# Kernel optimization log

Hardware: AMD Instinct MI355X
Metric: run time of the kernel (lower is better)

Reference implementation:

```python
import jax, jax.numpy as jnp
import numpy as np

W = 8       # token width
H = 2       # attention heads
NC = 1024   # number of cycles
L = 256     # darts per cycle
CLAMP = 10000.0


def _safe(x, clamp=CLAMP):
    x = jnp.nan_to_num(x, nan=0.0, posinf=clamp, neginf=-clamp)
    return jnp.clip(x, -clamp, clamp)


def _safe_softmax(logits, axis):
    w = jax.nn.softmax(_safe(logits), axis=axis)
    w = jnp.nan_to_num(w, nan=0.0, posinf=0.0, neginf=0.0)
    denom = jnp.maximum(w.sum(axis=axis, keepdims=True), 1e-6)
    return w / denom


def _layernorm(x, g, b, eps=1e-5):
    mu = x.mean(-1, keepdims=True)
    var = x.var(-1, keepdims=True)  # biased, matches torch LayerNorm
    return (x - mu) * jax.lax.rsqrt(var + eps) * g + b


def _mha(x, in_w, in_b, out_w, out_b, n_heads, mask=None):
    # torch nn.MultiheadAttention (batch_first) semantics. x: [B,S,E]
    B, S, E = x.shape
    d = E // n_heads
    qkv = x @ in_w.T + in_b
    q, k, v = jnp.split(qkv, 3, axis=-1)
    q = q.reshape(B, S, n_heads, d)
    k = k.reshape(B, S, n_heads, d)
    v = v.reshape(B, S, n_heads, d)
    scores = jnp.einsum('bshd,bthd->bhst', q, k) / jnp.sqrt(jnp.asarray(d, x.dtype))
    if mask is not None:
        scores = scores + mask  # broadcast [S,S] over batch/heads
    attn = jax.nn.softmax(scores, axis=-1)
    out = jnp.einsum('bhst,bthd->bshd', attn, v).reshape(B, S, E)
    return out @ out_w.T + out_b


def _cycle_mask(length):
    m = jnp.full((length, length), -1e9, dtype=jnp.float32)
    i = jnp.arange(length)
    m = m.at[i, i].set(0.0)
    m = m.at[i, (i - 1) % length].set(0.0)
    m = m.at[i, (i + 1) % length].set(0.0)
    return m


def _normalize_orientation(darts):
    # darts: [L,2]; polygon vertices are cumulative sums (origin first, last dart dropped)
    verts = jnp.concatenate([jnp.zeros((1, 2), darts.dtype), jnp.cumsum(darts[:-1], axis=0)], axis=0)
    x, y = verts[:, 0], verts[:, 1]
    area = 0.5 * jnp.sum(x * jnp.roll(y, -1) - y * jnp.roll(x, -1))
    return jnp.where(area >= 0.0, darts, jnp.flip(-darts, axis=0))


def setup_inputs() -> dict:
    key = jax.random.key(0)
    ks = jax.random.split(key, 32)
    def p(i, shape, s=0.2):
        return jax.random.normal(ks[i], shape, jnp.float32) * s
    return {
        'dart_features': jax.random.normal(ks[0], (NC, L, 3), jnp.float32),
        # dart_embed Linear(3,W)
        'de_w': p(1, (W, 3)), 'de_b': p(2, (W,)),
        # cycle_attn MultiheadAttention(W, 2)
        'ca_in_w': p(3, (3 * W, W)), 'ca_in_b': p(4, (3 * W,)),
        'ca_out_w': p(5, (W, W)), 'ca_out_b': p(6, (W,)),
        # cycle_norm
        'cn_g': jnp.ones((W,), jnp.float32), 'cn_b': jnp.zeros((W,), jnp.float32),
        # cycle_score Linear(W,1)
        'cs_w': p(7, (1, W)), 'cs_b': p(8, (1,)),
        # cycle_pool_proj: LN, Linear, ReLU, Linear
        'cp_ln_g': jnp.ones((W,), jnp.float32), 'cp_ln_b': jnp.zeros((W,), jnp.float32),
        'cp_w1': p(9, (W, W)), 'cp_b1': p(10, (W,)),
        'cp_w2': p(11, (W, W)), 'cp_b2': p(12, (W,)),
        # inter_cycle_attn
        'ia_in_w': p(13, (3 * W, W)), 'ia_in_b': p(14, (3 * W,)),
        'ia_out_w': p(15, (W, W)), 'ia_out_b': p(16, (W,)),
        # inter_cycle_norm
        'in_g': jnp.ones((W,), jnp.float32), 'in_b': jnp.zeros((W,), jnp.float32),
        # inter_cycle_score
        'is_w': p(17, (1, W)), 'is_b': p(18, (1,)),
        # token_proj: LN, Linear, ReLU, Linear
        'tp_ln_g': jnp.ones((W,), jnp.float32), 'tp_ln_b': jnp.zeros((W,), jnp.float32),
        'tp_w1': p(19, (W, W)), 'tp_b1': p(20, (W,)),
        'tp_w2': p(21, (W, W)), 'tp_b2': p(22, (W,)),
    }


def reference(dart_features, de_w, de_b, ca_in_w, ca_in_b, ca_out_w, ca_out_b,
              cn_g, cn_b, cs_w, cs_b, cp_ln_g, cp_ln_b, cp_w1, cp_b1, cp_w2, cp_b2,
              ia_in_w, ia_in_b, ia_out_w, ia_out_b, in_g, in_b, is_w, is_b,
              tp_ln_g, tp_ln_b, tp_w1, tp_b1, tp_w2, tp_b2):
    nc, ln, _ = dart_features.shape
    # ---- encode_cycle, vectorized over all cycles ----
    xy = jax.vmap(_normalize_orientation)(dart_features[..., :2])          # [C,L,2]
    nrm = jnp.linalg.norm(xy, axis=-1, keepdims=True)
    feats = _safe(jnp.concatenate([xy, nrm], axis=-1))                     # [C,L,3]
    emb = _safe(jax.nn.relu(feats @ de_w.T + de_b))                        # [C,L,W]
    mask = _cycle_mask(ln)
    attn = _mha(emb, ca_in_w, ca_in_b, ca_out_w, ca_out_b, H, mask)
    emb = _safe(_layernorm(_safe(emb + attn), cn_g, cn_b))                 # [C,L,W]
    logits = _safe((emb @ cs_w.T + cs_b)[..., 0])                          # [C,L]
    wts = _safe_softmax(logits, axis=1)
    pooled = jnp.sum(emb * wts[..., None], axis=1)                         # [C,W]
    hpool = _layernorm(pooled, cp_ln_g, cp_ln_b)
    cyc = _safe(jax.nn.relu(hpool @ cp_w1.T + cp_b1) @ cp_w2.T + cp_b2)    # [C,W]
    # ---- tokenize_collection ----
    coll = _safe(cyc)[None]                                                # [1,C,W]
    attn2 = _mha(coll, ia_in_w, ia_in_b, ia_out_w, ia_out_b, H)
    coll = _safe(_layernorm(_safe(coll + attn2), in_g, in_b))[0]           # [C,W]
    lg = _safe((coll @ is_w.T + is_b)[..., 0])                             # [C]
    w2 = _safe_softmax(lg, axis=0)
    tok_in = jnp.sum(coll * w2[:, None], axis=0)                           # [W]
    h2 = _layernorm(tok_in, tp_ln_g, tp_ln_b)
    token = _safe(jax.nn.relu(h2 @ tp_w1.T + tp_b1) @ tp_w2.T + tp_b2)     # [W]
    return token
```

## Files before the change

### kernel.cpp

```cpp
#include <hip/hip_runtime.h>
#include <math.h>

#define FCLAMP 10000.0f
#define NCYC 1024
#define NB2 (NCYC / 4)

__device__ __forceinline__ float safef(float x) {
    if (isnan(x)) return 0.0f;
    return fmaxf(fminf(x, FCLAMP), -FCLAMP);
}

__device__ __forceinline__ float wsum_b(float v) {
#pragma unroll
    for (int m = 1; m <= 32; m <<= 1) v += __shfl_xor(v, m, 64);
    return v;
}
__device__ __forceinline__ float wmax_b(float v) {
#pragma unroll
    for (int m = 1; m <= 32; m <<= 1) v = fmaxf(v, __shfl_xor(v, m, 64));
    return v;
}

__global__ __launch_bounds__(64, 1) void k_cycle(
    const float* __restrict__ df,
    const float* __restrict__ de_w, const float* __restrict__ de_b,
    const float* __restrict__ ca_in_w, const float* __restrict__ ca_in_b,
    const float* __restrict__ ca_out_w, const float* __restrict__ ca_out_b,
    const float* __restrict__ cn_g, const float* __restrict__ cn_b,
    const float* __restrict__ cs_w, const float* __restrict__ cs_b,
    const float* __restrict__ cp_ln_g, const float* __restrict__ cp_ln_b,
    const float* __restrict__ cp_w1, const float* __restrict__ cp_b1,
    const float* __restrict__ cp_w2, const float* __restrict__ cp_b2,
    const float* __restrict__ ia_in_w, const float* __restrict__ ia_in_b,
    float* __restrict__ ws_cyc,
    float* __restrict__ ws_q,
    float* __restrict__ ws_kT,
    float* __restrict__ ws_vT,
    unsigned* __restrict__ ws_cnt)
{
    const int lane = threadIdx.x;
    const int nc   = blockIdx.x;
    if (nc == 0 && lane == 0) *ws_cnt = 0u;

    const float* base = df + (size_t)nc * 768 + lane * 12;
    const float4 A = *(const float4*)(base);
    const float4 B = *(const float4*)(base + 4);
    const float4 C = *(const float4*)(base + 8);
    float dxr[4] = {A.x, A.w, B.z, C.y};
    float dyr[4] = {A.y, B.x, B.w, C.z};

    float sx[4], sy[4];
    sx[0] = dxr[0]; sy[0] = dyr[0];
#pragma unroll
    for (int r = 1; r < 4; ++r) { sx[r] = sx[r - 1] + dxr[r]; sy[r] = sy[r - 1] + dyr[r]; }
    const float tx = sx[3], ty = sy[3];
    float ixs = tx, iys = ty;
#pragma unroll
    for (int off = 1; off < 64; off <<= 1) {
        const float ax = __shfl_up(ixs, off, 64);
        const float ay = __shfl_up(iys, off, 64);
        if (lane >= off) { ixs += ax; iys += ay; }
    }
    const float bx = ixs - tx, by = iys - ty;

    float cc = 0.f;
#pragma unroll
    for (int r = 0; r < 4; ++r) {
        const float vx = bx + (r ? sx[r - 1] : 0.f);
        const float vy = by + (r ? sy[r - 1] : 0.f);
        if ((lane * 4 + r) < 255) cc += vx * dyr[r] - vy * dxr[r];
    }
    const float area2 = wsum_b(cc);

    if (!(area2 >= 0.f)) {
        float nx[4], ny[4];
#pragma unroll
        for (int r = 0; r < 4; ++r) {
            nx[r] = -__shfl(dxr[3 - r], 63 - lane, 64);
            ny[r] = -__shfl(dyr[3 - r], 63 - lane, 64);
        }
#pragma unroll
        for (int r = 0; r < 4; ++r) { dxr[r] = nx[r]; dyr[r] = ny[r]; }
    }

    float embA[4][8];
#pragma unroll
    for (int r = 0; r < 4; ++r) {
        const float fx = safef(dxr[r]);
        const float fy = safef(dyr[r]);
        const float fn = safef(sqrtf(dxr[r] * dxr[r] + dyr[r] * dyr[r]));
#pragma unroll
        for (int j = 0; j < 8; ++j) {
            const float e = de_b[j] + fx * de_w[j * 3] + fy * de_w[j * 3 + 1] + fn * de_w[j * 3 + 2];
            embA[r][j] = safef(fmaxf(e, 0.f));
        }
    }

    float qA[4][8], kA[4][8], vA[4][8];
#pragma unroll
    for (int r = 0; r < 4; ++r) {
#pragma unroll
        for (int o = 0; o < 24; ++o) {
            float val = ca_in_b[o];
#pragma unroll
            for (int k = 0; k < 8; ++k) val += embA[r][k] * ca_in_w[o * 8 + k];
            if (o < 8)       qA[r][o] = val;
            else if (o < 16) kA[r][o - 8] = val;
            else             vA[r][o - 16] = val;
        }
    }

    const int lprev = (lane + 63) & 63, lnext = (lane + 1) & 63;
    float kp[8], kn[8], vp[8], vn[8];
#pragma unroll
    for (int d = 0; d < 8; ++d) {
        kp[d] = __shfl(kA[3][d], lprev, 64);
        kn[d] = __shfl(kA[0][d], lnext, 64);
        vp[d] = __shfl(vA[3][d], lprev, 64);
        vn[d] = __shfl(vA[0][d], lnext, 64);
    }

    float lgr[4];
#pragma unroll
    for (int r = 0; r < 4; ++r) {
        float kprev[8], knext[8], vprev[8], vnext[8];
#pragma unroll
        for (int d = 0; d < 8; ++d) {
            kprev[d] = (r == 0) ? kp[d] : kA[r - 1][d];
            knext[d] = (r == 3) ? kn[d] : kA[r + 1][d];
            vprev[d] = (r == 0) ? vp[d] : vA[r - 1][d];
            vnext[d] = (r == 3) ? vn[d] : vA[r + 1][d];
        }
        float att[8];
#pragma unroll
        for (int h = 0; h < 2; ++h) {
            float s0 = 0.f, s1 = 0.f, s2 = 0.f;
#pragma unroll
            for (int d = 0; d < 4; ++d) {
                const float qv = qA[r][h * 4 + d];
                s0 += qv * kprev[h * 4 + d];
                s1 += qv * kA[r][h * 4 + d];
                s2 += qv * knext[h * 4 + d];
            }
            s0 *= 0.5f; s1 *= 0.5f; s2 *= 0.5f;
            const float m  = fmaxf(s0, fmaxf(s1, s2));
            const float e0 = __expf(s0 - m), e1 = __expf(s1 - m), e2 = __expf(s2 - m);
            const float inv = 1.f / (e0 + e1 + e2);
#pragma unroll
            for (int d = 0; d < 4; ++d)
                att[h * 4 + d] = (e0 * vprev[h * 4 + d] + e1 * vA[r][h * 4 + d] +
                                  e2 * vnext[h * 4 + d]) * inv;
        }
        float x8[8];
#pragma unroll
        for (int j = 0; j < 8; ++j) {
            float ao = ca_out_b[j];
#pragma unroll
            for (int k = 0; k < 8; ++k) ao += att[k] * ca_out_w[j * 8 + k];
            x8[j] = safef(embA[r][j] + ao);
        }
        float mu = 0.f;
#pragma unroll
        for (int j = 0; j < 8; ++j) mu += x8[j];
        mu *= 0.125f;
        float var = 0.f;
#pragma unroll
        for (int j = 0; j < 8; ++j) { const float d = x8[j] - mu; var += d * d; }
        var *= 0.125f;
        const float rs = rsqrtf(var + 1e-5f);
        float lg = cs_b[0];
#pragma unroll
        for (int j = 0; j < 8; ++j) {
            embA[r][j] = safef((x8[j] - mu) * rs * cn_g[j] + cn_b[j]);
            lg += embA[r][j] * cs_w[j];
        }
        lgr[r] = safef(lg);
    }

    float M = fmaxf(fmaxf(lgr[0], lgr[1]), fmaxf(lgr[2], lgr[3]));
    M = wmax_b(M);
    float er[4], esum = 0.f;
#pragma unroll
    for (int r = 0; r < 4; ++r) { er[r] = __expf(lgr[r] - M); esum += er[r]; }
    const float S = wsum_b(esum);
    const float invS = 1.f / S;
    float pool[8];
#pragma unroll
    for (int j = 0; j < 8; ++j) {
        float pj = er[0] * embA[0][j] + er[1] * embA[1][j] + er[2] * embA[2][j] + er[3] * embA[3][j];
        pool[j] = wsum_b(pj) * invS;
    }

    float mu2 = 0.f;
#pragma unroll
    for (int j = 0; j < 8; ++j) mu2 += pool[j];
    mu2 *= 0.125f;
    float v2 = 0.f;
#pragma unroll
    for (int j = 0; j < 8; ++j) { const float d = pool[j] - mu2; v2 += d * d; }
    const float rs2 = rsqrtf(v2 * 0.125f + 1e-5f);
    float hh[8];
#pragma unroll
    for (int j = 0; j < 8; ++j) hh[j] = (pool[j] - mu2) * rs2 * cp_ln_g[j] + cp_ln_b[j];
    float r1[8];
#pragma unroll
    for (int j = 0; j < 8; ++j) {
        float a = cp_b1[j];
#pragma unroll
        for (int k = 0; k < 8; ++k) a += hh[k] * cp_w1[j * 8 + k];
        r1[j] = fmaxf(a, 0.f);
    }
    float cy[8];
#pragma unroll
    for (int j = 0; j < 8; ++j) {
        float a = cp_b2[j];
#pragma unroll
        for (int k = 0; k < 8; ++k) a += r1[k] * cp_w2[j * 8 + k];
        cy[j] = safef(a);
    }
    if (lane == 0) {
        *(float4*)(ws_cyc + nc * 8)     = make_float4(cy[0], cy[1], cy[2], cy[3]);
        *(float4*)(ws_cyc + nc * 8 + 4) = make_float4(cy[4], cy[5], cy[6], cy[7]);
    }

    if (lane < 24) {
        const float* wrow = ia_in_w + lane * 8;
        float g2 = ia_in_b[lane];
#pragma unroll
        for (int k = 0; k < 8; ++k) g2 += cy[k] * wrow[k];
        if (lane < 8)       ws_q[nc * 8 + lane] = g2;
        else if (lane < 16) ws_kT[(lane - 8) * NCYC + nc] = g2;
        else                ws_vT[(lane - 16) * NCYC + nc] = g2;
    }
}

__global__ __launch_bounds__(256) void k_attn_final(
    const float* __restrict__ ws_cyc,
    const float* __restrict__ ws_q,
    const float* __restrict__ ws_kT,
    const float* __restrict__ ws_vT,
    const float* __restrict__ ia_out_w, const float* __restrict__ ia_out_b,
    const float* __restrict__ in_g, const float* __restrict__ in_b,
    const float* __restrict__ is_w, const float* __restrict__ is_b,
    const float* __restrict__ tp_ln_g, const float* __restrict__ tp_ln_b,
    const float* __restrict__ tp_w1, const float* __restrict__ tp_b1,
    const float* __restrict__ tp_w2, const float* __restrict__ tp_b2,
    float* __restrict__ ws_coll,
    float* __restrict__ ws_lg,
    unsigned* __restrict__ ws_cnt,
    float* __restrict__ out)
{
    __shared__ float sredM[4], sredS[4], spool[4][8];
    __shared__ unsigned s_last;

    const int lane = threadIdx.x & 63;
    const int wid  = threadIdx.x >> 6;
    const int g    = blockIdx.x * 4 + wid;

    float q[8];
#pragma unroll
    for (int d = 0; d < 8; ++d) q[d] = 0.5f * ws_q[g * 8 + d];

    float sc0[16], sc1[16];
    float m0 = -1e30f, m1 = -1e30f;
#pragma unroll
    for (int j = 0; j < 4; ++j) {
        const int t4 = j * 256 + lane * 4;
        float s0[4] = {0, 0, 0, 0}, s1[4] = {0, 0, 0, 0};
#pragma unroll
        for (int d = 0; d < 8; ++d) {
            const float4 kv = *(const float4*)(ws_kT + d * NCYC + t4);
            const float qd = q[d];
            float* s = (d < 4) ? s0 : s1;
            s[0] += qd * kv.x; s[1] += qd * kv.y; s[2] += qd * kv.z; s[3] += qd * kv.w;
        }
#pragma unroll
        for (int c = 0; c < 4; ++c) {
            sc0[j * 4 + c] = s0[c]; sc1[j * 4 + c] = s1[c];
            m0 = fmaxf(m0, s0[c]); m1 = fmaxf(m1, s1[c]);
        }
    }
    m0 = wmax_b(m0); m1 = wmax_b(m1);

    float l0 = 0.f, l1 = 0.f;
    float a0[4] = {0, 0, 0, 0}, a1[4] = {0, 0, 0, 0};
#pragma unroll
    for (int j = 0; j < 4; ++j) {
        const int t4 = j * 256 + lane * 4;
        float e0[4], e1[4];
#pragma unroll
        for (int c = 0; c < 4; ++c) {
            e0[c] = __expf(sc0[j * 4 + c] - m0);
            e1[c] = __expf(sc1[j * 4 + c] - m1);
            l0 += e0[c]; l1 += e1[c];
        }
#pragma unroll
        for (int d = 0; d < 4; ++d) {
            const float4 v0 = *(const float4*)(ws_vT + d * NCYC + t4);
            const float4 v1 = *(const float4*)(ws_vT + (4 + d) * NCYC + t4);
            a0[d] += e0[0] * v0.x + e0[1] * v0.y + e0[2] * v0.z + e0[3] * v0.w;
            a1[d] += e1[0] * v1.x + e1[1] * v1.y + e1[2] * v1.z + e1[3] * v1.w;
        }
    }
    l0 = wsum_b(l0); l1 = wsum_b(l1);
#pragma unroll
    for (int d = 0; d < 4; ++d) { a0[d] = wsum_b(a0[d]); a1[d] = wsum_b(a1[d]); }

    float attn8[8];
#pragma unroll
    for (int d = 0; d < 4; ++d) { attn8[d] = a0[d] / l0; attn8[4 + d] = a1[d] / l1; }

    const float4 cyA = *(const float4*)(ws_cyc + g * 8);
    const float4 cyB = *(const float4*)(ws_cyc + g * 8 + 4);
    const float cyc[8] = {cyA.x, cyA.y, cyA.z, cyA.w, cyB.x, cyB.y, cyB.z, cyB.w};
    float x8[8];
#pragma unroll
    for (int j = 0; j < 8; ++j) {
        float ao = ia_out_b[j];
#pragma unroll
        for (int k = 0; k < 8; ++k) ao += attn8[k] * ia_out_w[j * 8 + k];
        x8[j] = safef(cyc[j] + ao);
    }
    float mu = 0.f;
#pragma unroll
    for (int j = 0; j < 8; ++j) mu += x8[j];
    mu *= 0.125f;
    float var = 0.f;
#pragma unroll
    for (int j = 0; j < 8; ++j) { const float d = x8[j] - mu; var += d * d; }
    var *= 0.125f;
    const float rs = rsqrtf(var + 1e-5f);
    float lgv = is_b[0];
    float cl8[8];
#pragma unroll
    for (int j = 0; j < 8; ++j) {
        cl8[j] = safef((x8[j] - mu) * rs * in_g[j] + in_b[j]);
        lgv += cl8[j] * is_w[j];
    }
    if (lane == 0) {
        *(float4*)(ws_coll + g * 8)     = make_float4(cl8[0], cl8[1], cl8[2], cl8[3]);
        *(float4*)(ws_coll + g * 8 + 4) = make_float4(cl8[4], cl8[5], cl8[6], cl8[7]);
        ws_lg[g] = safef(lgv);
    }

    __syncthreads();
    if (threadIdx.x == 0) {
        __threadfence();
        const unsigned old = atomicAdd(ws_cnt, 1u);
        s_last = (old == NB2 - 1) ? 1u : 0u;
    }
    __syncthreads();
    if (!s_last) return;
    __threadfence();

    const int tid = threadIdx.x;
    float lgv4[4], cl[4][8];
#pragma unroll
    for (int r = 0; r < 4; ++r) {
        const int t = tid + 256 * r;
        lgv4[r] = ws_lg[t];
        const float4 u = *(const float4*)(ws_coll + t * 8);
        const float4 w = *(const float4*)(ws_coll + t * 8 + 4);
        cl[r][0] = u.x; cl[r][1] = u.y; cl[r][2] = u.z; cl[r][3] = u.w;
        cl[r][4] = w.x; cl[r][5] = w.y; cl[r][6] = w.z; cl[r][7] = w.w;
    }
    float m = fmaxf(fmaxf(lgv4[0], lgv4[1]), fmaxf(lgv4[2], lgv4[3]));
    m = wmax_b(m);
    if (lane == 0) sredM[wid] = m;
    __syncthreads();
    const float M = fmaxf(fmaxf(sredM[0], sredM[1]), fmaxf(sredM[2], sredM[3]));
    float er[4], es = 0.f;
#pragma unroll
    for (int r = 0; r < 4; ++r) { er[r] = __expf(lgv4[r] - M); es += er[r]; }
    es = wsum_b(es);
    if (lane == 0) sredS[wid] = es;
#pragma unroll
    for (int j = 0; j < 8; ++j) {
        float pj = er[0] * cl[0][j] + er[1] * cl[1][j] + er[2] * cl[2][j] + er[3] * cl[3][j];
        pj = wsum_b(pj);
        if (lane == 0) spool[wid][j] = pj;
    }
    __syncthreads();

    if (wid == 0) {
        const float S = sredS[0] + sredS[1] + sredS[2] + sredS[3];
        const float invS = 1.f / S;
        float pool[8];
#pragma unroll
        for (int j = 0; j < 8; ++j)
            pool[j] = (spool[0][j] + spool[1][j] + spool[2][j] + spool[3][j]) * invS;
        float mu2 = 0.f;
#pragma unroll
        for (int j = 0; j < 8; ++j) mu2 += pool[j];
        mu2 *= 0.125f;
        float v2 = 0.f;
#pragma unroll
        for (int j = 0; j < 8; ++j) { const float d = pool[j] - mu2; v2 += d * d; }
        const float rs2 = rsqrtf(v2 * 0.125f + 1e-5f);
        float hh[8];
#pragma unroll
        for (int j = 0; j < 8; ++j) hh[j] = (pool[j] - mu2) * rs2 * tp_ln_g[j] + tp_ln_b[j];
        float r1[8];
#pragma unroll
        for (int j = 0; j < 8; ++j) {
            float a = tp_b1[j];
#pragma unroll
            for (int k = 0; k < 8; ++k) a += hh[k] * tp_w1[j * 8 + k];
            r1[j] = fmaxf(a, 0.f);
        }
        if (lane == 0) {
#pragma unroll
            for (int j = 0; j < 8; ++j) {
                float a = tp_b2[j];
#pragma unroll
                for (int k = 0; k < 8; ++k) a += r1[k] * tp_w2[j * 8 + k];
                out[j] = safef(a);
            }
        }
    }
}

extern "C" void kernel_launch(void* const* d_in, const int* in_sizes, int n_in,
                              void* d_out, int out_size, void* d_ws, size_t ws_size,
                              hipStream_t stream) {
    const float* df       = (const float*)d_in[0];
    const float* de_w     = (const float*)d_in[1];
    const float* de_b     = (const float*)d_in[2];
    const float* ca_in_w  = (const float*)d_in[3];
    const float* ca_in_b  = (const float*)d_in[4];
    const float* ca_out_w = (const float*)d_in[5];
    const float* ca_out_b = (const float*)d_in[6];
    const float* cn_g     = (const float*)d_in[7];
    const float* cn_b     = (const float*)d_in[8];
    const float* cs_w     = (const float*)d_in[9];
    const float* cs_b     = (const float*)d_in[10];
    const float* cp_ln_g  = (const float*)d_in[11];
    const float* cp_ln_b  = (const float*)d_in[12];
    const float* cp_w1    = (const float*)d_in[13];
    const float* cp_b1    = (const float*)d_in[14];
    const float* cp_w2    = (const float*)d_in[15];
    const float* cp_b2    = (const float*)d_in[16];
    const float* ia_in_w  = (const float*)d_in[17];
    const float* ia_in_b  = (const float*)d_in[18];
    const float* ia_out_w = (const float*)d_in[19];
    const float* ia_out_b = (const float*)d_in[20];
    const float* in_g     = (const float*)d_in[21];
    const float* in_b     = (const float*)d_in[22];
    const float* is_w     = (const float*)d_in[23];
    const float* is_b     = (const float*)d_in[24];
    const float* tp_ln_g  = (const float*)d_in[25];
    const float* tp_ln_b  = (const float*)d_in[26];
    const float* tp_w1    = (const float*)d_in[27];
    const float* tp_b1    = (const float*)d_in[28];
    const float* tp_w2    = (const float*)d_in[29];
    const float* tp_b2    = (const float*)d_in[30];

    float* ws      = (float*)d_ws;
    float* ws_cyc  = ws;
    float* ws_q    = ws + NCYC * 8;
    float* ws_kT   = ws + NCYC * 16;
    float* ws_vT   = ws + NCYC * 24;
    float* ws_coll = ws + NCYC * 32;
    float* ws_lg   = ws + NCYC * 40;
    unsigned* ws_cnt = (unsigned*)(ws + NCYC * 41);

    k_cycle<<<NCYC, 64, 0, stream>>>(
        df, de_w, de_b, ca_in_w, ca_in_b, ca_out_w, ca_out_b,
        cn_g, cn_b, cs_w, cs_b, cp_ln_g, cp_ln_b,
        cp_w1, cp_b1, cp_w2, cp_b2, ia_in_w, ia_in_b,
        ws_cyc, ws_q, ws_kT, ws_vT, ws_cnt);

    k_attn_final<<<NB2, 256, 0, stream>>>(
        ws_cyc, ws_q, ws_kT, ws_vT, ia_out_w, ia_out_b, in_g, in_b, is_w, is_b,
        tp_ln_g, tp_ln_b, tp_w1, tp_b1, tp_w2, tp_b2,
        ws_coll, ws_lg, ws_cnt, (float*)d_out);
}
```

Measured before the change: 149.0 us.

## Fuse both stages into one cooperative kernel with grid syncs

Merges the per-cycle kernel and the collection-attention/final-reduction kernel into a single cooperative launch of 1024 single-wave blocks. Two grid-wide barriers replace the second kernel launch and the atomic last-block counter. The collection attention is now computed by one 64-lane wave per query instead of the previous 256-thread blocks, and block 0 alone does the final softmax pooling and MLP. This removes one launch boundary but adds grid-sync costs and requires all 1024 blocks to be co-resident.

After: 391.5 us. 163% more time.

```diff
diff --git a/kernel.cpp b/kernel.cpp
--- a/kernel.cpp
+++ b/kernel.cpp
@@ -1,9 +1,11 @@
 #include <hip/hip_runtime.h>
+#include <hip/hip_cooperative_groups.h>
 #include <math.h>
+
+namespace cg = cooperative_groups;
 
 #define FCLAMP 10000.0f
 #define NCYC 1024
-#define NB2 (NCYC / 4)
 
 __device__ __forceinline__ float safef(float x) {
     if (isnan(x)) return 0.0f;
@@ -21,143 +23,297 @@
     return v;
 }
 
-__global__ __launch_bounds__(64, 1) void k_cycle(
-    const float* __restrict__ df,
-    const float* __restrict__ de_w, const float* __restrict__ de_b,
-    const float* __restrict__ ca_in_w, const float* __restrict__ ca_in_b,
-    const float* __restrict__ ca_out_w, const float* __restrict__ ca_out_b,
-    const float* __restrict__ cn_g, const float* __restrict__ cn_b,
-    const float* __restrict__ cs_w, const float* __restrict__ cs_b,
-    const float* __restrict__ cp_ln_g, const float* __restrict__ cp_ln_b,
-    const float* __restrict__ cp_w1, const float* __restrict__ cp_b1,
-    const float* __restrict__ cp_w2, const float* __restrict__ cp_b2,
-    const float* __restrict__ ia_in_w, const float* __restrict__ ia_in_b,
-    float* __restrict__ ws_cyc,
-    float* __restrict__ ws_q,
-    float* __restrict__ ws_kT,
-    float* __restrict__ ws_vT,
-    unsigned* __restrict__ ws_cnt)
-{
+struct Params {
+    const float* df;
+    const float* de_w;  const float* de_b;
+    const float* ca_in_w;  const float* ca_in_b;
+    const float* ca_out_w; const float* ca_out_b;
+    const float* cn_g;  const float* cn_b;
+    const float* cs_w;  const float* cs_b;
+    const float* cp_ln_g; const float* cp_ln_b;
+    const float* cp_w1; const float* cp_b1;
+    const float* cp_w2; const float* cp_b2;
+    const float* ia_in_w;  const float* ia_in_b;
+    const float* ia_out_w; const float* ia_out_b;
+    const float* in_g;  const float* in_b;
+    const float* is_w;  const float* is_b;
+    const float* tp_ln_g; const float* tp_ln_b;
+    const float* tp_w1; const float* tp_b1;
+    const float* tp_w2; const float* tp_b2;
+    float* ws_cyc;
+    float* ws_q;
+    float* ws_kT;
+    float* ws_vT;
+    float* ws_coll;
+    float* ws_lg;
+    float* out;
+};
+
+__global__ __launch_bounds__(64, 1) void k_all(Params p) {
     const int lane = threadIdx.x;
     const int nc   = blockIdx.x;
-    if (nc == 0 && lane == 0) *ws_cnt = 0u;
-
-    const float* base = df + (size_t)nc * 768 + lane * 12;
-    const float4 A = *(const float4*)(base);
-    const float4 B = *(const float4*)(base + 4);
-    const float4 C = *(const float4*)(base + 8);
-    float dxr[4] = {A.x, A.w, B.z, C.y};
-    float dyr[4] = {A.y, B.x, B.w, C.z};
-
-    float sx[4], sy[4];
-    sx[0] = dxr[0]; sy[0] = dyr[0];
-#pragma unroll
-    for (int r = 1; r < 4; ++r) { sx[r] = sx[r - 1] + dxr[r]; sy[r] = sy[r - 1] + dyr[r]; }
-    const float tx = sx[3], ty = sy[3];
-    float ixs = tx, iys = ty;
-#pragma unroll
-    for (int off = 1; off < 64; off <<= 1) {
-        const float ax = __shfl_up(ixs, off, 64);
-        const float ay = __shfl_up(iys, off, 64);
-        if (lane >= off) { ixs += ax; iys += ay; }
+
+    {
+        const float* base = p.df + (size_t)nc * 768 + lane * 12;
+        const float4 A = *(const float4*)(base);
+        const float4 B = *(const float4*)(base + 4);
+        const float4 C = *(const float4*)(base + 8);
+        float dxr[4] = {A.x, A.w, B.z, C.y};
+        float dyr[4] = {A.y, B.x, B.w, C.z};
+
+        float sx[4], sy[4];
+        sx[0] = dxr[0]; sy[0] = dyr[0];
+#pragma unroll
+        for (int r = 1; r < 4; ++r) { sx[r] = sx[r - 1] + dxr[r]; sy[r] = sy[r - 1] + dyr[r]; }
+        const float tx = sx[3], ty = sy[3];
+        float ixs = tx, iys = ty;
+#pragma unroll
+        for (int off = 1; off < 64; off <<= 1) {
+            const float ax = __shfl_up(ixs, off, 64);
+            const float ay = __shfl_up(iys, off, 64);
+            if (lane >= off) { ixs += ax; iys += ay; }
+        }
+        const float bx = ixs - tx, by = iys - ty;
+
+        float cc = 0.f;
+#pragma unroll
+        for (int r = 0; r < 4; ++r) {
+            const float vx = bx + (r ? sx[r - 1] : 0.f);
+            const float vy = by + (r ? sy[r - 1] : 0.f);
+            if ((lane * 4 + r) < 255) cc += vx * dyr[r] - vy * dxr[r];
+        }
+        const float area2 = wsum_b(cc);
+
+        if (!(area2 >= 0.f)) {
+            float nx[4], ny[4];
+#pragma unroll
+            for (int r = 0; r < 4; ++r) {
+                nx[r] = -__shfl(dxr[3 - r], 63 - lane, 64);
+                ny[r] = -__shfl(dyr[3 - r], 63 - lane, 64);
+            }
+#pragma unroll
+            for (int r = 0; r < 4; ++r) { dxr[r] = nx[r]; dyr[r] = ny[r]; }
+        }
+
+        float embA[4][8];
+#pragma unroll
+        for (int r = 0; r < 4; ++r) {
+            const float fx = safef(dxr[r]);
+            const float fy = safef(dyr[r]);
+            const float fn = safef(sqrtf(dxr[r] * dxr[r] + dyr[r] * dyr[r]));
+#pragma unroll
+            for (int j = 0; j < 8; ++j) {
+                const float e = p.de_b[j] + fx * p.de_w[j * 3] + fy * p.de_w[j * 3 + 1]
+                              + fn * p.de_w[j * 3 + 2];
+                embA[r][j] = safef(fmaxf(e, 0.f));
+            }
+        }
+
+        float qA[4][8], kA[4][8], vA[4][8];
+#pragma unroll
+        for (int r = 0; r < 4; ++r) {
+#pragma unroll
+            for (int o = 0; o < 24; ++o) {
+                float val = p.ca_in_b[o];
+#pragma unroll
+                for (int k = 0; k < 8; ++k) val += embA[r][k] * p.ca_in_w[o * 8 + k];
+                if (o < 8)       qA[r][o] = val;
+                else if (o < 16) kA[r][o - 8] = val;
+                else             vA[r][o - 16] = val;
+            }
+        }
+
+        const int lprev = (lane + 63) & 63, lnext = (lane + 1) & 63;
+        float kp[8], kn[8], vp[8], vn[8];
+#pragma unroll
+        for (int d = 0; d < 8; ++d) {
+            kp[d] = __shfl(kA[3][d], lprev, 64);
+            kn[d] = __shfl(kA[0][d], lnext, 64);
+            vp[d] = __shfl(vA[3][d], lprev, 64);
+            vn[d] = __shfl(vA[0][d], lnext, 64);
+        }
+
+        float lgr[4];
+#pragma unroll
+        for (int r = 0; r < 4; ++r) {
+            float kprev[8], knext[8], vprev[8], vnext[8];
+#pragma unroll
+            for (int d = 0; d < 8; ++d) {
+                kprev[d] = (r == 0) ? kp[d] : kA[r - 1][d];
+                knext[d] = (r == 3) ? kn[d] : kA[r + 1][d];
+                vprev[d] = (r == 0) ? vp[d] : vA[r - 1][d];
+                vnext[d] = (r == 3) ? vn[d] : vA[r + 1][d];
+            }
+            float att[8];
+#pragma unroll
+            for (int h = 0; h < 2; ++h) {
+                float s0 = 0.f, s1 = 0.f, s2 = 0.f;
+#pragma unroll
+                for (int d = 0; d < 4; ++d) {
+                    const float qv = qA[r][h * 4 + d];
+                    s0 += qv * kprev[h * 4 + d];
+                    s1 += qv * kA[r][h * 4 + d];
+                    s2 += qv * knext[h * 4 + d];
+                }
+                s0 *= 0.5f; s1 *= 0.5f; s2 *= 0.5f;
+                const float m  = fmaxf(s0, fmaxf(s1, s2));
+                const float e0 = __expf(s0 - m), e1 = __expf(s1 - m), e2 = __expf(s2 - m);
+                const float inv = 1.f / (e0 + e1 + e2);
+#pragma unroll
+                for (int d = 0; d < 4; ++d)
+                    att[h * 4 + d] = (e0 * vprev[h * 4 + d] + e1 * vA[r][h * 4 + d] +
+                                      e2 * vnext[h * 4 + d]) * inv;
+            }
+            float x8[8];
+#pragma unroll
+            for (int j = 0; j < 8; ++j) {
+                float ao = p.ca_out_b[j];
+#pragma unroll
+                for (int k = 0; k < 8; ++k) ao += att[k] * p.ca_out_w[j * 8 + k];
+                x8[j] = safef(embA[r][j] + ao);
+            }
+            float mu = 0.f;
+#pragma unroll
+            for (int j = 0; j < 8; ++j) mu += x8[j];
+            mu *= 0.125f;
+            float var = 0.f;
+#pragma unroll
+            for (int j = 0; j < 8; ++j) { const float d = x8[j] - mu; var += d * d; }
+            var *= 0.125f;
+            const float rs = rsqrtf(var + 1e-5f);
+            float lg = p.cs_b[0];
+#pragma unroll
+            for (int j = 0; j < 8; ++j) {
+                embA[r][j] = safef((x8[j] - mu) * rs * p.cn_g[j] + p.cn_b[j]);
+                lg += embA[r][j] * p.cs_w[j];
+            }
+            lgr[r] = safef(lg);
+        }
+
+        float M = fmaxf(fmaxf(lgr[0], lgr[1]), fmaxf(lgr[2], lgr[3]));
+        M = wmax_b(M);
+        float er[4], esum = 0.f;
+#pragma unroll
+        for (int r = 0; r < 4; ++r) { er[r] = __expf(lgr[r] - M); esum += er[r]; }
+        const float S = wsum_b(esum);
+        const float invS = 1.f / S;
+        float pool[8];
+#pragma unroll
+        for (int j = 0; j < 8; ++j) {
+            float pj = er[0] * embA[0][j] + er[1] * embA[1][j]
+                     + er[2] * embA[2][j] + er[3] * embA[3][j];
+            pool[j] = wsum_b(pj) * invS;
+        }
+
+        float mu2 = 0.f;
+#pragma unroll
+        for (int j = 0; j < 8; ++j) mu2 += pool[j];
+        mu2 *= 0.125f;
+        float v2 = 0.f;
+#pragma unroll
+        for (int j = 0; j < 8; ++j) { const float d = pool[j] - mu2; v2 += d * d; }
+        const float rs2 = rsqrtf(v2 * 0.125f + 1e-5f);
+        float hh[8];
+#pragma unroll
+        for (int j = 0; j < 8; ++j) hh[j] = (pool[j] - mu2) * rs2 * p.cp_ln_g[j] + p.cp_ln_b[j];
+        float r1[8];
+#pragma unroll
+        for (int j = 0; j < 8; ++j) {
+            float a = p.cp_b1[j];
+#pragma unroll
+            for (int k = 0; k < 8; ++k) a += hh[k] * p.cp_w1[j * 8 + k];
+            r1[j] = fmaxf(a, 0.f);
+        }
+        float cy[8];
+#pragma unroll
+        for (int j = 0; j < 8; ++j) {
+            float a = p.cp_b2[j];
+#pragma unroll
+            for (int k = 0; k < 8; ++k) a += r1[k] * p.cp_w2[j * 8 + k];
+            cy[j] = safef(a);
+        }
+        if (lane == 0) {
+            *(float4*)(p.ws_cyc + nc * 8)     = make_float4(cy[0], cy[1], cy[2], cy[3]);
+            *(float4*)(p.ws_cyc + nc * 8 + 4) = make_float4(cy[4], cy[5], cy[6], cy[7]);
+        }
+        if (lane < 24) {
+            const float* wrow = p.ia_in_w + lane * 8;
+            float g2 = p.ia_in_b[lane];
+#pragma unroll
+            for (int k = 0; k < 8; ++k) g2 += cy[k] * wrow[k];
+            if (lane < 8)       p.ws_q[nc * 8 + lane] = g2;
+            else if (lane < 16) p.ws_kT[(lane - 8) * NCYC + nc] = g2;
+            else                p.ws_vT[(lane - 16) * NCYC + nc] = g2;
+        }
     }
-    const float bx = ixs - tx, by = iys - ty;
-
-    float cc = 0.f;
-#pragma unroll
-    for (int r = 0; r < 4; ++r) {
-        const float vx = bx + (r ? sx[r - 1] : 0.f);
-        const float vy = by + (r ? sy[r - 1] : 0.f);
-        if ((lane * 4 + r) < 255) cc += vx * dyr[r] - vy * dxr[r];
-    }
-    const float area2 = wsum_b(cc);
-
-    if (!(area2 >= 0.f)) {
-        float nx[4], ny[4];
-#pragma unroll
-        for (int r = 0; r < 4; ++r) {
-            nx[r] = -__shfl(dxr[3 - r], 63 - lane, 64);
-            ny[r] = -__shfl(dyr[3 - r], 63 - lane, 64);
-        }
-#pragma unroll
-        for (int r = 0; r < 4; ++r) { dxr[r] = nx[r]; dyr[r] = ny[r]; }
-    }
-
-    float embA[4][8];
-#pragma unroll
-    for (int r = 0; r < 4; ++r) {
-        const float fx = safef(dxr[r]);
-        const float fy = safef(dyr[r]);
-        const float fn = safef(sqrtf(dxr[r] * dxr[r] + dyr[r] * dyr[r]));
-#pragma unroll
-        for (int j = 0; j < 8; ++j) {
-            const float e = de_b[j] + fx * de_w[j * 3] + fy * de_w[j * 3 + 1] + fn * de_w[j * 3 + 2];
-            embA[r][j] = safef(fmaxf(e, 0.f));
-        }
-    }
-
-    float qA[4][8], kA[4][8], vA[4][8];
-#pragma unroll
-    for (int r = 0; r < 4; ++r) {
-#pragma unroll
-        for (int o = 0; o < 24; ++o) {
-            float val = ca_in_b[o];
-#pragma unroll
-            for (int k = 0; k < 8; ++k) val += embA[r][k] * ca_in_w[o * 8 + k];
-            if (o < 8)       qA[r][o] = val;
-            else if (o < 16) kA[r][o - 8] = val;
-            else             vA[r][o - 16] = val;
-        }
-    }
-
-    const int lprev = (lane + 63) & 63, lnext = (lane + 1) & 63;
-    float kp[8], kn[8], vp[8], vn[8];
-#pragma unroll
-    for (int d = 0; d < 8; ++d) {
-        kp[d] = __shfl(kA[3][d], lprev, 64);
-        kn[d] = __shfl(kA[0][d], lnext, 64);
-        vp[d] = __shfl(vA[3][d], lprev, 64);
-        vn[d] = __shfl(vA[0][d], lnext, 64);
-    }
-
-    float lgr[4];
-#pragma unroll
-    for (int r = 0; r < 4; ++r) {
-        float kprev[8], knext[8], vprev[8], vnext[8];
-#pragma unroll
-        for (int d = 0; d < 8; ++d) {
-            kprev[d] = (r == 0) ? kp[d] : kA[r - 1][d];
-            knext[d] = (r == 3) ? kn[d] : kA[r + 1][d];
-            vprev[d] = (r == 0) ? vp[d] : vA[r - 1][d];
-            vnext[d] = (r == 3) ? vn[d] : vA[r + 1][d];
-        }
-        float att[8];
-#pragma unroll
-        for (int h = 0; h < 2; ++h) {
-            float s0 = 0.f, s1 = 0.f, s2 = 0.f;
+
+    cg::this_grid().sync();
+
+    {
+        const int g = nc;
+        float q[8];
+#pragma unroll
+        for (int d = 0; d < 8; ++d) q[d] = 0.5f * p.ws_q[g * 8 + d];
+
+        float sc0[16], sc1[16];
+        float m0 = -1e30f, m1 = -1e30f;
+#pragma unroll
+        for (int j = 0; j < 4; ++j) {
+            const int t4 = j * 256 + lane * 4;
+            float s0[4] = {0, 0, 0, 0}, s1[4] = {0, 0, 0, 0};
+#pragma unroll
+            for (int d = 0; d < 8; ++d) {
+                const float4 kv = *(const float4*)(p.ws_kT + d * NCYC + t4);
+                const float qd = q[d];
+                float* s = (d < 4) ? s0 : s1;
+                s[0] += qd * kv.x; s[1] += qd * kv.y; s[2] += qd * kv.z; s[3] += qd * kv.w;
+            }
+#pragma unroll
+            for (int c = 0; c < 4; ++c) {
+                sc0[j * 4 + c] = s0[c]; sc1[j * 4 + c] = s1[c];
+                m0 = fmaxf(m0, s0[c]); m1 = fmaxf(m1, s1[c]);
+            }
+        }
+        m0 = wmax_b(m0); m1 = wmax_b(m1);
+
+        float l0 = 0.f, l1 = 0.f;
+        float a0[4] = {0, 0, 0, 0}, a1[4] = {0, 0, 0, 0};
+#pragma unroll
+        for (int j = 0; j < 4; ++j) {
+            const int t4 = j * 256 + lane * 4;
+            float e0[4], e1[4];
+#pragma unroll
+            for (int c = 0; c < 4; ++c) {
+                e0[c] = __expf(sc0[j * 4 + c] - m0);
+                e1[c] = __expf(sc1[j * 4 + c] - m1);
+                l0 += e0[c]; l1 += e1[c];
+            }
 #pragma unroll
             for (int d = 0; d < 4; ++d) {
-                const float qv = qA[r][h * 4 + d];
-                s0 += qv * kprev[h * 4 + d];
-                s1 += qv * kA[r][h * 4 + d];
-                s2 += qv * knext[h * 4 + d];
-            }
-            s0 *= 0.5f; s1 *= 0.5f; s2 *= 0.5f;
-            const float m  = fmaxf(s0, fmaxf(s1, s2));
-            const float e0 = __expf(s0 - m), e1 = __expf(s1 - m), e2 = __expf(s2 - m);
-            const float inv = 1.f / (e0 + e1 + e2);
-#pragma unroll
-            for (int d = 0; d < 4; ++d)
-                att[h * 4 + d] = (e0 * vprev[h * 4 + d] + e1 * vA[r][h * 4 + d] +
-                                  e2 * vnext[h * 4 + d]) * inv;
-        }
+                const float4 v0 = *(const float4*)(p.ws_vT + d * NCYC + t4);
+                const float4 v1 = *(const float4*)(p.ws_vT + (4 + d) * NCYC + t4);
+                a0[d] += e0[0] * v0.x + e0[1] * v0.y + e0[2] * v0.z + e0[3] * v0.w;
+                a1[d] += e1[0] * v1.x + e1[1] * v1.y + e1[2] * v1.z + e1[3] * v1.w;
+            }
+        }
+        l0 = wsum_b(l0); l1 = wsum_b(l1);
+#pragma unroll
+        for (int d = 0; d < 4; ++d) { a0[d] = wsum_b(a0[d]); a1[d] = wsum_b(a1[d]); }
+
+        float attn8[8];
+#pragma unroll
+        for (int d = 0; d < 4; ++d) { attn8[d] = a0[d] / l0; attn8[4 + d] = a1[d] / l1; }
+
+        const float4 cyA = *(const float4*)(p.ws_cyc + g * 8);
+        const float4 cyB = *(const float4*)(p.ws_cyc + g * 8 + 4);
+        const float cyc[8] = {cyA.x, cyA.y, cyA.z, cyA.w, cyB.x, cyB.y, cyB.z, cyB.w};
         float x8[8];
 #pragma unroll
         for (int j = 0; j < 8; ++j) {
-            float ao = ca_out_b[j];
-#pragma unroll
-            for (int k = 0; k < 8; ++k) ao += att[k] * ca_out_w[j * 8 + k];
-            x8[j] = safef(embA[r][j] + ao);
+            float ao = p.ia_out_b[j];
+#pragma unroll
+            for (int k = 0; k < 8; ++k) ao += attn8[k] * p.ia_out_w[j * 8 + k];
+            x8[j] = safef(cyc[j] + ao);
         }
         float mu = 0.f;
 #pragma unroll
@@ -168,227 +324,49 @@
         for (int j = 0; j < 8; ++j) { const float d = x8[j] - mu; var += d * d; }
         var *= 0.125f;
         const float rs = rsqrtf(var + 1e-5f);
-        float lg = cs_b[0];
-#pragma unroll
-        for (int j = 0; j < 8; ++j) {
-            embA[r][j] = safef((x8[j] - mu) * rs * cn_g[j] + cn_b[j]);
-            lg += embA[r][j] * cs_w[j];
-        }
-        lgr[r] = safef(lg);
+        float lgv = p.is_b[0];
+        float cl8[8];
+#pragma unroll
+        for (int j = 0; j < 8; ++j) {
+            cl8[j] = safef((x8[j] - mu) * rs * p.in_g[j] + p.in_b[j]);
+            lgv += cl8[j] * p.is_w[j];
+        }
+        if (lane == 0) {
+            *(float4*)(p.ws_coll + g * 8)     = make_float4(cl8[0], cl8[1], cl8[2], cl8[3]);
+            *(float4*)(p.ws_coll + g * 8 + 4) = make_float4(cl8[4], cl8[5], cl8[6], cl8[7]);
+            p.ws_lg[g] = safef(lgv);
+        }
     }
 
-    float M = fmaxf(fmaxf(lgr[0], lgr[1]), fmaxf(lgr[2], lgr[3]));
-    M = wmax_b(M);
-    float er[4], esum = 0.f;
-#pragma unroll
-    for (int r = 0; r < 4; ++r) { er[r] = __expf(lgr[r] - M); esum += er[r]; }
-    const float S = wsum_b(esum);
-    const float invS = 1.f / S;
-    float pool[8];
-#pragma unroll
-    for (int j = 0; j < 8; ++j) {
-        float pj = er[0] * embA[0][j] + er[1] * embA[1][j] + er[2] * embA[2][j] + er[3] * embA[3][j];
-        pool[j] = wsum_b(pj) * invS;
-    }
-
-    float mu2 = 0.f;
-#pragma unroll
-    for (int j = 0; j < 8; ++j) mu2 += pool[j];
-    mu2 *= 0.125f;
-    float v2 = 0.f;
-#pragma unroll
-    for (int j = 0; j < 8; ++j) { const float d = pool[j] - mu2; v2 += d * d; }
-    const float rs2 = rsqrtf(v2 * 0.125f + 1e-5f);
-    float hh[8];
-#pragma unroll
-    for (int j = 0; j < 8; ++j) hh[j] = (pool[j] - mu2) * rs2 * cp_ln_g[j] + cp_ln_b[j];
-    float r1[8];
-#pragma unroll
-    for (int j = 0; j < 8; ++j) {
-        float a = cp_b1[j];
-#pragma unroll
-        for (int k = 0; k < 8; ++k) a += hh[k] * cp_w1[j * 8 + k];
-        r1[j] = fmaxf(a, 0.f);
-    }
-    float cy[8];
-#pragma unroll
-    for (int j = 0; j < 8; ++j) {
-        float a = cp_b2[j];
-#pragma unroll
-        for (int k = 0; k < 8; ++k) a += r1[k] * cp_w2[j * 8 + k];
-        cy[j] = safef(a);
-    }
-    if (lane == 0) {
-        *(float4*)(ws_cyc + nc * 8)     = make_float4(cy[0], cy[1], cy[2], cy[3]);
-        *(float4*)(ws_cyc + nc * 8 + 4) = make_float4(cy[4], cy[5], cy[6], cy[7]);
-    }
-
-    if (lane < 24) {
-        const float* wrow = ia_in_w + lane * 8;
-        float g2 = ia_in_b[lane];
-#pragma unroll
-        for (int k = 0; k < 8; ++k) g2 += cy[k] * wrow[k];
-        if (lane < 8)       ws_q[nc * 8 + lane] = g2;
-        else if (lane < 16) ws_kT[(lane - 8) * NCYC + nc] = g2;
-        else                ws_vT[(lane - 16) * NCYC + nc] = g2;
-    }
-}
-
-__global__ __launch_bounds__(256) void k_attn_final(
-    const float* __restrict__ ws_cyc,
-    const float* __restrict__ ws_q,
-    const float* __restrict__ ws_kT,
-    const float* __restrict__ ws_vT,
-    const float* __restrict__ ia_out_w, const float* __restrict__ ia_out_b,
-    const float* __restrict__ in_g, const float* __restrict__ in_b,
-    const float* __restrict__ is_w, const float* __restrict__ is_b,
-    const float* __restrict__ tp_ln_g, const float* __restrict__ tp_ln_b,
-    const float* __restrict__ tp_w1, const float* __restrict__ tp_b1,
-    const float* __restrict__ tp_w2, const float* __restrict__ tp_b2,
-    float* __restrict__ ws_coll,
-    float* __restrict__ ws_lg,
-    unsigned* __restrict__ ws_cnt,
-    float* __restrict__ out)
-{
-    __shared__ float sredM[4], sredS[4], spool[4][8];
-    __shared__ unsigned s_last;
-
-    const int lane = threadIdx.x & 63;
-    const int wid  = threadIdx.x >> 6;
-    const int g    = blockIdx.x * 4 + wid;
-
-    float q[8];
-#pragma unroll
-    for (int d = 0; d < 8; ++d) q[d] = 0.5f * ws_q[g * 8 + d];
-
-    float sc0[16], sc1[16];
-    float m0 = -1e30f, m1 = -1e30f;
-#pragma unroll
-    for (int j = 0; j < 4; ++j) {
-        const int t4 = j * 256 + lane * 4;
-        float s0[4] = {0, 0, 0, 0}, s1[4] = {0, 0, 0, 0};
-#pragma unroll
-        for (int d = 0; d < 8; ++d) {
-            const float4 kv = *(const float4*)(ws_kT + d * NCYC + t4);
-            const float qd = q[d];
-            float* s = (d < 4) ? s0 : s1;
-            s[0] += qd * kv.x; s[1] += qd * kv.y; s[2] += qd * kv.z; s[3] += qd * kv.w;
-        }
-#pragma unroll
-        for (int c = 0; c < 4; ++c) {
-            sc0[j * 4 + c] = s0[c]; sc1[j * 4 + c] = s1[c];
-            m0 = fmaxf(m0, s0[c]); m1 = fmaxf(m1, s1[c]);
-        }
-    }
-    m0 = wmax_b(m0); m1 = wmax_b(m1);
-
-    float l0 = 0.f, l1 = 0.f;
-    float a0[4] = {0, 0, 0, 0}, a1[4] = {0, 0, 0, 0};
-#pragma unroll
-    for (int j = 0; j < 4; ++j) {
-        const int t4 = j * 256 + lane * 4;
-        float e0[4], e1[4];
-#pragma unroll
-        for (int c = 0; c < 4; ++c) {
-            e0[c] = __expf(sc0[j * 4 + c] - m0);
-            e1[c] = __expf(sc1[j * 4 + c] - m1);
-            l0 += e0[c]; l1 += e1[c];
-        }
-#pragma unroll
-        for (int d = 0; d < 4; ++d) {
-            const float4 v0 = *(const float4*)(ws_vT + d * NCYC + t4);
-            const float4 v1 = *(const float4*)(ws_vT + (4 + d) * NCYC + t4);
-            a0[d] += e0[0] * v0.x + e0[1] * v0.y + e0[2] * v0.z + e0[3] * v0.w;
-            a1[d] += e1[0] * v1.x + e1[1] * v1.y + e1[2] * v1.z + e1[3] * v1.w;
-        }
-    }
-    l0 = wsum_b(l0); l1 = wsum_b(l1);
-#pragma unroll
-    for (int d = 0; d < 4; ++d) { a0[d] = wsum_b(a0[d]); a1[d] = wsum_b(a1[d]); }
-
-    float attn8[8];
-#pragma unroll
-    for (int d = 0; d < 4; ++d) { attn8[d] = a0[d] / l0; attn8[4 + d] = a1[d] / l1; }
-
-    const float4 cyA = *(const float4*)(ws_cyc + g * 8);
-    const float4 cyB = *(const float4*)(ws_cyc + g * 8 + 4);
-    const float cyc[8] = {cyA.x, cyA.y, cyA.z, cyA.w, cyB.x, cyB.y, cyB.z, cyB.w};
-    float x8[8];
-#pragma unroll
-    for (int j = 0; j < 8; ++j) {
-        float ao = ia_out_b[j];
-#pragma unroll
-        for (int k = 0; k < 8; ++k) ao += attn8[k] * ia_out_w[j * 8 + k];
-        x8[j] = safef(cyc[j] + ao);
-    }
-    float mu = 0.f;
-#pragma unroll
-    for (int j = 0; j < 8; ++j) mu += x8[j];
-    mu *= 0.125f;
-    float var = 0.f;
-#pragma unroll
-    for (int j = 0; j < 8; ++j) { const float d = x8[j] - mu; var += d * d; }
-    var *= 0.125f;
-    const float rs = rsqrtf(var + 1e-5f);
-    float lgv = is_b[0];
-    float cl8[8];
-#pragma unroll
-    for (int j = 0; j < 8; ++j) {
-        cl8[j] = safef((x8[j] - mu) * rs * in_g[j] + in_b[j]);
-        lgv += cl8[j] * is_w[j];
-    }
-    if (lane == 0) {
-        *(float4*)(ws_coll + g * 8)     = make_float4(cl8[0], cl8[1], cl8[2], cl8[3]);
-        *(float4*)(ws_coll + g * 8 + 4) = make_float4(cl8[4], cl8[5], cl8[6], cl8[7]);
-        ws_lg[g] = safef(lgv);
-    }
-
-    __syncthreads();
-    if (threadIdx.x == 0) {
-        __threadfence();
-        const unsigned old = atomicAdd(ws_cnt, 1u);
-        s_last = (old == NB2 - 1) ? 1u : 0u;
-    }
-    __syncthreads();
-    if (!s_last) return;
-    __threadfence();
-
-    const int tid = threadIdx.x;
-    float lgv4[4], cl[4][8];
-#pragma unroll
-    for (int r = 0; r < 4; ++r) {
-        const int t = tid + 256 * r;
-        lgv4[r] = ws_lg[t];
-        const float4 u = *(const float4*)(ws_coll + t * 8);
-        const float4 w = *(const float4*)(ws_coll + t * 8 + 4);
-        cl[r][0] = u.x; cl[r][1] = u.y; cl[r][2] = u.z; cl[r][3] = u.w;
-        cl[r][4] = w.x; cl[r][5] = w.y; cl[r][6] = w.z; cl[r][7] = w.w;
-    }
-    float m = fmaxf(fmaxf(lgv4[0], lgv4[1]), fmaxf(lgv4[2], lgv4[3]));
-    m = wmax_b(m);
-    if (lane == 0) sredM[wid] = m;
-    __syncthreads();
-    const float M = fmaxf(fmaxf(sredM[0], sredM[1]), fmaxf(sredM[2], sredM[3]));
-    float er[4], es = 0.f;
-#pragma unroll
-    for (int r = 0; r < 4; ++r) { er[r] = __expf(lgv4[r] - M); es += er[r]; }
-    es = wsum_b(es);
-    if (lane == 0) sredS[wid] = es;
-#pragma unroll
-    for (int j = 0; j < 8; ++j) {
-        float pj = er[0] * cl[0][j] + er[1] * cl[1][j] + er[2] * cl[2][j] + er[3] * cl[3][j];
-        pj = wsum_b(pj);
-        if (lane == 0) spool[wid][j] = pj;
-    }
-    __syncthreads();
-
-    if (wid == 0) {
-        const float S = sredS[0] + sredS[1] + sredS[2] + sredS[3];
+    cg::this_grid().sync();
+
+    if (nc == 0) {
+        float lg16[16];
+        float mloc = -1e30f;
+#pragma unroll
+        for (int j = 0; j < 16; ++j) {
+            lg16[j] = p.ws_lg[j * 64 + lane];
+            mloc = fmaxf(mloc, lg16[j]);
+        }
+        const float M = wmax_b(mloc);
+        float er16[16], es = 0.f;
+        float acc[8] = {0, 0, 0, 0, 0, 0, 0, 0};
+#pragma unroll
+        for (int j = 0; j < 16; ++j) {
+            const float e = __expf(lg16[j] - M);
+            er16[j] = e; es += e;
+            const int t = j * 64 + lane;
+            const float4 u = *(const float4*)(p.ws_coll + t * 8);
+            const float4 w = *(const float4*)(p.ws_coll + t * 8 + 4);
+            acc[0] += e * u.x; acc[1] += e * u.y; acc[2] += e * u.z; acc[3] += e * u.w;
+            acc[4] += e * w.x; acc[5] += e * w.y; acc[6] += e * w.z; acc[7] += e * w.w;
+        }
+        const float S = wsum_b(es);
         const float invS = 1.f / S;
         float pool[8];
 #pragma unroll
-        for (int j = 0; j < 8; ++j)
-            pool[j] = (spool[0][j] + spool[1][j] + spool[2][j] + spool[3][j]) * invS;
+        for (int j = 0; j < 8; ++j) pool[j] = wsum_b(acc[j]) * invS;
+
         float mu2 = 0.f;
 #pragma unroll
         for (int j = 0; j < 8; ++j) mu2 += pool[j];
@@ -399,22 +377,22 @@
         const float rs2 = rsqrtf(v2 * 0.125f + 1e-5f);
         float hh[8];
 #pragma unroll
-        for (int j = 0; j < 8; ++j) hh[j] = (pool[j] - mu2) * rs2 * tp_ln_g[j] + tp_ln_b[j];
+        for (int j = 0; j < 8; ++j) hh[j] = (pool[j] - mu2) * rs2 * p.tp_ln_g[j] + p.tp_ln_b[j];
         float r1[8];
 #pragma unroll
         for (int j = 0; j < 8; ++j) {
-            float a = tp_b1[j];
-#pragma unroll
-            for (int k = 0; k < 8; ++k) a += hh[k] * tp_w1[j * 8 + k];
+            float a = p.tp_b1[j];
+#pragma unroll
+            for (int k = 0; k < 8; ++k) a += hh[k] * p.tp_w1[j * 8 + k];
             r1[j] = fmaxf(a, 0.f);
         }
         if (lane == 0) {
 #pragma unroll
             for (int j = 0; j < 8; ++j) {
-                float a = tp_b2[j];
-#pragma unroll
-                for (int k = 0; k < 8; ++k) a += r1[k] * tp_w2[j * 8 + k];
-                out[j] = safef(a);
+                float a = p.tp_b2[j];
+#pragma unroll
+                for (int k = 0; k < 8; ++k) a += r1[k] * p.tp_w2[j * 8 + k];
+                p.out[j] = safef(a);
             }
         }
     }
@@ -423,55 +401,50 @@
 extern "C" void kernel_launch(void* const* d_in, const int* in_sizes, int n_in,
                               void* d_out, int out_size, void* d_ws, size_t ws_size,
                               hipStream_t stream) {
-    const float* df       = (const float*)d_in[0];
-    const float* de_w     = (const float*)d_in[1];
-    const float* de_b     = (const float*)d_in[2];
-    const float* ca_in_w  = (const float*)d_in[3];
-    const float* ca_in_b  = (const float*)d_in[4];
-    const float* ca_out_w = (const float*)d_in[5];
-    const float* ca_out_b = (const float*)d_in[6];
-    const float* cn_g     = (const float*)d_in[7];
-    const float* cn_b     = (const float*)d_in[8];
-    const float* cs_w     = (const float*)d_in[9];
-    const float* cs_b     = (const float*)d_in[10];
-    const float* cp_ln_g  = (const float*)d_in[11];
-    const float* cp_ln_b  = (const float*)d_in[12];
-    const float* cp_w1    = (const float*)d_in[13];
-    const float* cp_b1    = (const float*)d_in[14];
-    const float* cp_w2    = (const float*)d_in[15];
-    const float* cp_b2    = (const float*)d_in[16];
-    const float* ia_in_w  = (const float*)d_in[17];
-    const float* ia_in_b  = (const float*)d_in[18];
-    const float* ia_out_w = (const float*)d_in[19];
-    const float* ia_out_b = (const float*)d_in[20];
-    const float* in_g     = (const float*)d_in[21];
-    const float* in_b     = (const float*)d_in[22];
-    const float* is_w     = (const float*)d_in[23];
-    const float* is_b     = (const float*)d_in[24];
-    const float* tp_ln_g  = (const float*)d_in[25];
-    const float* tp_ln_b  = (const float*)d_in[26];
-    const float* tp_w1    = (const float*)d_in[27];
-    const float* tp_b1    = (const float*)d_in[28];
-    const float* tp_w2    = (const float*)d_in[29];
-    const float* tp_b2    = (const float*)d_in[30];
-
-    float* ws      = (float*)d_ws;
-    float* ws_cyc  = ws;
-    float* ws_q    = ws + NCYC * 8;
-    float* ws_kT   = ws + NCYC * 16;
-    float* ws_vT   = ws + NCYC * 24;
-    float* ws_coll = ws + NCYC * 32;
-    float* ws_lg   = ws + NCYC * 40;
-    unsigned* ws_cnt = (unsigned*)(ws + NCYC * 41);
-
-    k_cycle<<<NCYC, 64, 0, stream>>>(
-        df, de_w, de_b, ca_in_w, ca_in_b, ca_out_w, ca_out_b,
-        cn_g, cn_b, cs_w, cs_b, cp_ln_g, cp_ln_b,
-        cp_w1, cp_b1, cp_w2, cp_b2, ia_in_w, ia_in_b,
-        ws_cyc, ws_q, ws_kT, ws_vT, ws_cnt);
-
-    k_attn_final<<<NB2, 256, 0, stream>>>(
-        ws_cyc, ws_q, ws_kT, ws_vT, ia_out_w, ia_out_b, in_g, in_b, is_w, is_b,
-        tp_ln_g, tp_ln_b, tp_w1, tp_b1, tp_w2, tp_b2,
-        ws_coll, ws_lg, ws_cnt, (float*)d_out);
+    float* ws = (float*)d_ws;
+
+    Params P;
+    P.df       = (const float*)d_in[0];
+    P.de_w     = (const float*)d_in[1];
+    P.de_b     = (const float*)d_in[2];
+    P.ca_in_w  = (const float*)d_in[3];
+    P.ca_in_b  = (const float*)d_in[4];
+    P.ca_out_w = (const float*)d_in[5];
+    P.ca_out_b = (const float*)d_in[6];
+    P.cn_g     = (const float*)d_in[7];
+    P.cn_b     = (const float*)d_in[8];
+    P.cs_w     = (const float*)d_in[9];
+    P.cs_b     = (const float*)d_in[10];
+    P.cp_ln_g  = (const float*)d_in[11];
+    P.cp_ln_b  = (const float*)d_in[12];
+    P.cp_w1    = (const float*)d_in[13];
+    P.cp_b1    = (const float*)d_in[14];
+    P.cp_w2    = (const float*)d_in[15];
+    P.cp_b2    = (const float*)d_in[16];
+    P.ia_in_w  = (const float*)d_in[17];
+    P.ia_in_b  = (const float*)d_in[18];
+    P.ia_out_w = (const float*)d_in[19];
+    P.ia_out_b = (const float*)d_in[20];
+    P.in_g     = (const float*)d_in[21];
+    P.in_b     = (const float*)d_in[22];
+    P.is_w     = (const float*)d_in[23];
+    P.is_b     = (const float*)d_in[24];
+    P.tp_ln_g  = (const float*)d_in[25];
+    P.tp_ln_b  = (const float*)d_in[26];
+    P.tp_w1    = (const float*)d_in[27];
+    P.tp_b1    = (const float*)d_in[28];
+    P.tp_w2    = (const float*)d_in[29];
+    P.tp_b2    = (const float*)d_in[30];
+
+    P.ws_cyc  = ws;
+    P.ws_q    = ws + NCYC * 8;
+    P.ws_kT   = ws + NCYC * 16;
+    P.ws_vT   = ws + NCYC * 24;
+    P.ws_coll = ws + NCYC * 32;
+    P.ws_lg   = ws + NCYC * 40;
+    P.out     = (float*)d_out;
+
+    void* kargs[] = { (void*)&P };
+    hipLaunchCooperativeKernel((const void*)k_all, dim3(NCYC), dim3(64),
+                               kargs, 0, stream);
 }
```
